# Kernel optimization log

Hardware: AMD Instinct MI355X
Metric: run time of the kernel (lower is better)

Reference implementation:

```python
import jax, jax.numpy as jnp
import numpy as np

BETA = 0.25
SCALE_NUM = 4  # len(latents_scale)


def setup_inputs() -> dict:
    key = jax.random.key(0)
    kz, ke = jax.random.split(key)
    z = jax.random.normal(kz, (8, 256, 32, 32), dtype=jnp.float32)
    emb_weight = jax.random.normal(ke, (16384, 256), dtype=jnp.float32) * 0.02
    return {"z": z, "emb_weight": emb_weight}


def reference(z, emb_weight):
    # z: [B, C, H, W] with C == vq_embed_dim and H == W (source reshapes with W twice)
    B, C, H, W = z.shape
    z_det = jax.lax.stop_gradient(z)

    # NOTE: in the source, `residual` is flattened ONCE before the scale loop and
    # never updated inside it, so every scale picks the same indices. We compute
    # the nearest-codebook assignment once (identical math, argmin of cdist is
    # invariant under sqrt, so squared distances suffice).
    residual = jnp.transpose(z_det, (0, 2, 3, 1)).reshape(-1, C)  # [N, D], N=B*H*W
    d2 = (jnp.sum(residual * residual, axis=1, keepdims=True)
          - 2.0 * residual @ emb_weight.T
          + jnp.sum(emb_weight * emb_weight, axis=1))  # [N, n_e]
    idx = jnp.argmin(d2, axis=1).reshape(B, W, W)  # [B, W, W]

    quantized = jnp.transpose(emb_weight[idx], (0, 3, 1, 2))  # [B, C, H, W]

    z_hat = jnp.zeros_like(z_det)
    loss = jnp.float32(0.0)
    for _ in range(SCALE_NUM):
        z_hat = z_hat + quantized
        loss = loss + BETA * jnp.mean((jax.lax.stop_gradient(z_hat) - z) ** 2) \
                    + jnp.mean((z_hat - z_det) ** 2)
    loss = loss / SCALE_NUM

    total_idx = jnp.concatenate([idx] * SCALE_NUM, axis=1)  # [B, SCALE_NUM*W, W]
    z_hat_out = z + jax.lax.stop_gradient(z_hat - z)  # straight-through
    return z_hat_out, loss, total_idx
```

## Files before the change

### kernel.cpp

```cpp
#include <hip/hip_runtime.h>

#define D      256
#define N_E    16384
#define NPTS   8192
#define ZOUT   2097152
#define MARGIN 2.0e-2f
#define STRIPS 4
#define ECH    17

typedef short bf16x8 __attribute__((ext_vector_type(8)));
typedef unsigned short us8 __attribute__((ext_vector_type(8)));
typedef float f32x16 __attribute__((ext_vector_type(16)));
typedef unsigned long long u64;

__device__ __forceinline__ unsigned short f2bf(float x) {
    unsigned int u = __float_as_uint(x);
    return (unsigned short)((u + 0x7FFFu + ((u >> 16) & 1u)) >> 16);
}
__device__ __forceinline__ float bf2f(unsigned short h) {
    return __uint_as_float((unsigned int)h << 16);
}
__device__ __forceinline__ void gl_lds16(const void* g, void* l) {
    __builtin_amdgcn_global_load_lds(
        (const __attribute__((address_space(1))) unsigned int*)g,
        (__attribute__((address_space(3))) unsigned int*)l, 16, 0, 0);
}

__global__ __launch_bounds__(256) void prep(
    const float* __restrict__ z, const float* __restrict__ emb,
    unsigned short* __restrict__ Zpk, float* __restrict__ Zf32,
    unsigned short* __restrict__ Epk, float* __restrict__ e2,
    float* __restrict__ loss) {
    __shared__ float sh[32];
    const int t = threadIdx.x;
    if (blockIdx.x == 0 && t == 0) loss[0] = 0.f;
    if (blockIdx.x < 256) {
        const int n0 = blockIdx.x * 32;
        const int p = t & 31, ks8 = t >> 5;
        const int n = n0 + p;
        const int b = n >> 10, hw = n & 1023;
        const float* zb = z + (size_t)b * 262144 + hw;
        const int k0 = ks8 * 32;
        float v[32];
        #pragma unroll
        for (int kk = 0; kk < 32; ++kk)
            v[kk] = zb[(size_t)(k0 + kk) * 1024];
        #pragma unroll
        for (int i = 0; i < 8; ++i) {
            float4 f = {v[i * 4], v[i * 4 + 1], v[i * 4 + 2], v[i * 4 + 3]};
            *(float4*)(Zf32 + (size_t)n * D + k0 + i * 4) = f;
        }
        const int g = n >> 5;
        #pragma unroll
        for (int i = 0; i < 4; ++i) {
            us8 hv;
            #pragma unroll
            for (int c = 0; c < 8; ++c) hv[c] = f2bf(-2.0f * v[i * 8 + c]);
            const int kabs = k0 + i * 8;
            const int ks = kabs >> 4;
            const int l = (n & 31) + ((kabs >> 3) & 1) * 32;
            *(us8*)(Zpk + ((size_t)(g * 16 + ks) * 64 + l) * 8) = hv;
        }
    } else {
        const int bi = blockIdx.x - 256;
        const int j0 = bi * 32;
        const int jj = j0 + (t >> 3), q = t & 7;
        const float* row = emb + (size_t)jj * D + q * 32;
        float v[32];
        float s = 0.f;
        #pragma unroll
        for (int i = 0; i < 8; ++i) {
            const float4 x = *(const float4*)(row + i * 4);
            v[i * 4] = x.x; v[i * 4 + 1] = x.y; v[i * 4 + 2] = x.z; v[i * 4 + 3] = x.w;
            s += x.x * x.x + x.y * x.y + x.z * x.z + x.w * x.w;
        }
        #pragma unroll
        for (int i = 0; i < 4; ++i) {
            us8 hv;
            #pragma unroll
            for (int c = 0; c < 8; ++c) hv[c] = f2bf(v[i * 8 + c]);
            const int kabs = q * 32 + i * 8;
            const int ks = kabs >> 4;
            const int l = (jj & 31) + ((kabs >> 3) & 1) * 32;
            *(us8*)(Epk + ((size_t)(bi * ECH + ks) * 64 + l) * 8) = hv;
        }
        s += __shfl_xor(s, 1);
        s += __shfl_xor(s, 2);
        s += __shfl_xor(s, 4);
        if (q == 0) { e2[jj] = s; sh[t >> 3] = s; }
        __syncthreads();
        if (t < 64) {
            us8 hv;
            #pragma unroll
            for (int c = 0; c < 8; ++c) hv[c] = 0;
            if (t < 32) {
                const float vv = sh[t];
                const unsigned short hi = f2bf(vv);
                hv[0] = hi;
                hv[1] = f2bf(vv - bf2f(hi));
            }
            *(us8*)(Epk + ((size_t)bi * ECH + 16) * 512 + t * 8) = hv;
        }
    }
}

__global__ __launch_bounds__(256, 2) void mfma_gemm(
    const unsigned short* __restrict__ Epk, const unsigned short* __restrict__ Zpk,
    float* __restrict__ tminv, u64* __restrict__ tmask) {
    __shared__ unsigned short Zbuf[64 * 512];

    const int tid = threadIdx.x, lane = tid & 63, wid = tid >> 6;
    const int c32 = lane & 31, l5 = lane >> 5;
    const int n0 = blockIdx.x * 128;
    const int cs0 = blockIdx.y * (STRIPS * 256);

    us8 puu;
    #pragma unroll
    for (int c = 0; c < 8; ++c) puu[c] = 0;
    if (l5 == 0) { puu[0] = 0x3F80; puu[1] = 0x3F80; }
    const bf16x8 pu = (bf16x8)puu;

    #pragma unroll
    for (int ks = 0; ks < 16; ++ks)
        gl_lds16(Zpk + ((size_t)((n0 >> 5) + wid) * 16 + ks) * 512 + lane * 8,
                 Zbuf + (wid * 16 + ks) * 512);
    __syncthreads();

    for (int s = 0; s < STRIPS; ++s) {
        const int cb = cs0 + s * 256 + wid * 64;
        const unsigned short* eb =
            Epk + ((size_t)(cb >> 5) * ECH) * 512 + lane * 8;
        const unsigned short* zb = Zbuf + lane * 8;

        f32x16 acc[2][4];
        const f32x16 z16 = {0.f};
        #pragma unroll
        for (int i = 0; i < 2; ++i)
            #pragma unroll
            for (int j = 0; j < 4; ++j) acc[i][j] = z16;

        bf16x8 eq0a = *(const bf16x8*)(eb);
        bf16x8 eq0b = *(const bf16x8*)(eb + ECH * 512);
        bf16x8 eq1a = *(const bf16x8*)(eb + 512);
        bf16x8 eq1b = *(const bf16x8*)(eb + ECH * 512 + 512);
        bf16x8 pc[4], pn[4];
        #pragma unroll
        for (int j = 0; j < 4; ++j) pc[j] = *(const bf16x8*)(zb + (j * 16) * 512);

        #pragma unroll 4
        for (int ks = 0; ks < 16; ++ks) {
            bf16x8 ef0, ef1;
            if ((ks & 1) == 0) { ef0 = eq0a; ef1 = eq0b; }
            else               { ef0 = eq1a; ef1 = eq1b; }
            if (ks < 15) {
                const unsigned short* ep = eb + (ks + 2) * 512;
                if ((ks & 1) == 0) {
                    eq0a = *(const bf16x8*)ep;
                    eq0b = *(const bf16x8*)(ep + ECH * 512);
                } else {
                    eq1a = *(const bf16x8*)ep;
                    eq1b = *(const bf16x8*)(ep + ECH * 512);
                }
                #pragma unroll
                for (int j = 0; j < 4; ++j)
                    pn[j] = *(const bf16x8*)(zb + (j * 16 + ks + 1) * 512);
            }
            acc[0][0] = __builtin_amdgcn_mfma_f32_32x32x16_bf16(ef0, pc[0], acc[0][0], 0, 0, 0);
            acc[0][1] = __builtin_amdgcn_mfma_f32_32x32x16_bf16(ef0, pc[1], acc[0][1], 0, 0, 0);
            acc[0][2] = __builtin_amdgcn_mfma_f32_32x32x16_bf16(ef0, pc[2], acc[0][2], 0, 0, 0);
            acc[0][3] = __builtin_amdgcn_mfma_f32_32x32x16_bf16(ef0, pc[3], acc[0][3], 0, 0, 0);
            acc[1][0] = __builtin_amdgcn_mfma_f32_32x32x16_bf16(ef1, pc[0], acc[1][0], 0, 0, 0);
            acc[1][1] = __builtin_amdgcn_mfma_f32_32x32x16_bf16(ef1, pc[1], acc[1][1], 0, 0, 0);
            acc[1][2] = __builtin_amdgcn_mfma_f32_32x32x16_bf16(ef1, pc[2], acc[1][2], 0, 0, 0);
            acc[1][3] = __builtin_amdgcn_mfma_f32_32x32x16_bf16(ef1, pc[3], acc[1][3], 0, 0, 0);
            if (ks < 15) {
                #pragma unroll
                for (int j = 0; j < 4; ++j) pc[j] = pn[j];
            }
        }
        #pragma unroll
        for (int j = 0; j < 4; ++j) {
            acc[0][j] = __builtin_amdgcn_mfma_f32_32x32x16_bf16(eq0a, pu, acc[0][j], 0, 0, 0);
            acc[1][j] = __builtin_amdgcn_mfma_f32_32x32x16_bf16(eq0b, pu, acc[1][j], 0, 0, 0);
        }

        #pragma unroll
        for (int j = 0; j < 4; ++j) {
            float m = acc[0][j][0];
            #pragma unroll
            for (int r = 1; r < 16; ++r) m = fminf(m, acc[0][j][r]);
            #pragma unroll
            for (int r = 0; r < 16; ++r) m = fminf(m, acc[1][j][r]);
            m = fminf(m, __shfl_xor(m, 32));
            const float th = m + MARGIN;
            unsigned mk[2];
            #pragma unroll
            for (int i = 0; i < 2; ++i) {
                unsigned mm = 0;
                #pragma unroll
                for (int r = 0; r < 16; ++r) {
                    const int row = (r & 3) + 8 * (r >> 2) + 4 * l5;
                    mm |= (acc[i][j][r] <= th) ? (1u << row) : 0u;
                }
                mk[i] = mm | (unsigned)__shfl_xor((int)mm, 32);
            }
            if (l5 == 0) {
                const size_t pt = (size_t)(n0 + j * 32 + c32);
                tminv[pt * 256 + (cb >> 6)] = m;
                tmask[pt * 256 + (cb >> 6)] = ((u64)mk[1] << 32) | (u64)mk[0];
            }
        }
    }
}

__global__ __launch_bounds__(1024) void rescore_quant(
    const float* __restrict__ tminv, const u64* __restrict__ tmask,
    const float* __restrict__ Zf32, const float* __restrict__ emb,
    const float* __restrict__ e2, const float* __restrict__ z,
    float* __restrict__ out, float* __restrict__ out_idx,
    float* __restrict__ loss) {
    __shared__ int idx_s[32];
    __shared__ float wsum[16];
    const int tid = threadIdx.x, lane = tid & 63, wd = tid >> 6;
    const int n0 = blockIdx.x * 32;
    const int b = n0 >> 10, hw0 = n0 & 1023;

    #pragma unroll 1
    for (int p = 0; p < 2; ++p) {
        const int lp = wd * 2 + p;
        const int n = n0 + lp;
        const float4 zr = *(const float4*)(Zf32 + (size_t)n * D + lane * 4);
        const float4 tv = *(const float4*)(tminv + (size_t)n * 256 + lane * 4);

        float m1 = fminf(fminf(tv.x, tv.y), fminf(tv.z, tv.w));
        #pragma unroll
        for (int st = 1; st < 64; st <<= 1) m1 = fminf(m1, __shfl_xor(m1, st));
        const float thresh = m1 + MARGIN;

        u64 best = ~0ull;
        const float tva[4] = {tv.x, tv.y, tv.z, tv.w};
        #pragma unroll
        for (int k = 0; k < 4; ++k) {
            u64 gm = __ballot(tva[k] <= thresh);
            while (gm) {
                const int bit = (int)__builtin_ctzll(gm);
                gm &= gm - 1;
                const int g = bit * 4 + k;
                u64 cm = tmask[(size_t)n * 256 + g];
                while (cm) {
                    const int r = (int)__builtin_ctzll(cm);
                    cm &= cm - 1;
                    const int c = g * 64 + r;
                    const float4 ev = *(const float4*)(emb + (size_t)c * D + lane * 4);
                    float s = zr.x * ev.x + zr.y * ev.y + zr.z * ev.z + zr.w * ev.w;
                    #pragma unroll
                    for (int st = 1; st < 64; st <<= 1) s += __shfl_xor(s, st);
                    const float d = e2[c] - 2.0f * s;
                    unsigned int u = __float_as_uint(d);
                    u = (u & 0x80000000u) ? ~u : (u | 0x80000000u);
                    const u64 key = ((u64)u << 32) | (unsigned int)c;
                    if (key < best) best = key;
                }
            }
        }
        if (lane == 0)
            idx_s[lp] = (int)(unsigned int)(best & 0xFFFFFFFFull);
    }
    __syncthreads();

    if (tid < 32) {
        const float fv = (float)idx_s[tid];
        #pragma unroll
        for (int sc = 0; sc < 4; ++sc)
            out_idx[b * 4096 + sc * 1024 + hw0 + tid] = fv;
    }
    const int hw_l = tid & 31, cg = tid >> 5;
    const int j = idx_s[hw_l];
    const float* er = emb + (size_t)j * D + cg * 8;
    const float4 q0 = *(const float4*)er;
    const float4 q1 = *(const float4*)(er + 4);
    const float qv[8] = {q0.x, q0.y, q0.z, q0.w, q1.x, q1.y, q1.z, q1.w};
    float e = 0.f;
    #pragma unroll
    for (int cc = 0; cc < 8; ++cc) {
        const int c = cg * 8 + cc;
        const size_t zi = (size_t)b * 262144 + (size_t)c * 1024 + hw0 + hw_l;
        const float zv = z[zi];
        const float q = qv[cc];
        const float zh = ((q + q) + q) + q;
        out[zi] = zv + (zh - zv);
        e += 30.0f * q * q - 20.0f * q * zv + 4.0f * zv * zv;
    }
    #pragma unroll
    for (int off = 32; off > 0; off >>= 1) e += __shfl_down(e, off);
    if (lane == 0) wsum[wd] = e;
    __syncthreads();
    if (tid == 0) {
        float s = 0.f;
        #pragma unroll
        for (int i = 0; i < 16; ++i) s += wsum[i];
        atomicAdd(loss, s * (0.3125f / 2097152.0f));
    }
}

extern "C" void kernel_launch(void* const* d_in, const int* in_sizes, int n_in,
                              void* d_out, int out_size, void* d_ws, size_t ws_size,
                              hipStream_t stream) {
    const float* z = (const float*)d_in[0];
    const float* emb = (const float*)d_in[1];
    float* out = (float*)d_out;

    unsigned short* Zpk = (unsigned short*)d_ws;
    unsigned short* Epk = Zpk + (size_t)NPTS * D;
    float* Zf32 = (float*)(Epk + (size_t)(N_E / 32) * ECH * 512);
    float* e2 = Zf32 + (size_t)NPTS * D;
    float* tminv = e2 + N_E;
    u64* tmask = (u64*)(tminv + (size_t)NPTS * 256);

    float* loss = out + ZOUT;
    float* out_idx = out + ZOUT + 1;

    prep<<<768, 256, 0, stream>>>(z, emb, Zpk, Zf32, Epk, e2, loss);
    mfma_gemm<<<dim3(NPTS / 128, N_E / (256 * STRIPS)), 256, 0, stream>>>(
        Epk, Zpk, tminv, tmask);
    rescore_quant<<<256, 1024, 0, stream>>>(tminv, tmask, Zf32, emb, e2, z,
                                            out, out_idx, loss);
}
```

Baseline: 161.6 us.

## Fuse GEMM and rescore kernels using a grid-wide atomic barrier

```diff
diff --git a/kernel.cpp b/kernel.cpp
--- a/kernel.cpp
+++ b/kernel.cpp
@@ -7,6 +7,7 @@
 #define MARGIN 2.0e-2f
 #define STRIPS 4
 #define ECH    17
+#define GRIDF  512
 
 typedef short bf16x8 __attribute__((ext_vector_type(8)));
 typedef unsigned short us8 __attribute__((ext_vector_type(8)));
@@ -30,10 +31,10 @@
     const float* __restrict__ z, const float* __restrict__ emb,
     unsigned short* __restrict__ Zpk, float* __restrict__ Zf32,
     unsigned short* __restrict__ Epk, float* __restrict__ e2,
-    float* __restrict__ loss) {
+    float* __restrict__ loss, unsigned int* __restrict__ cnt) {
     __shared__ float sh[32];
     const int t = threadIdx.x;
-    if (blockIdx.x == 0 && t == 0) loss[0] = 0.f;
+    if (blockIdx.x == 0 && t == 0) { loss[0] = 0.f; *cnt = 0u; }
     if (blockIdx.x < 256) {
         const int n0 = blockIdx.x * 32;
         const int p = t & 31, ks8 = t >> 5;
@@ -104,15 +105,22 @@
     }
 }
 
-__global__ __launch_bounds__(256, 2) void mfma_gemm(
+__global__ __launch_bounds__(256, 2) void gemm_fused(
     const unsigned short* __restrict__ Epk, const unsigned short* __restrict__ Zpk,
-    float* __restrict__ tminv, u64* __restrict__ tmask) {
+    float* __restrict__ tminv, u64* __restrict__ tmask,
+    const float* __restrict__ Zf32, const float* __restrict__ emb,
+    const float* __restrict__ e2, const float* __restrict__ z,
+    float* __restrict__ out, float* __restrict__ out_idx,
+    float* __restrict__ loss, unsigned int* __restrict__ cnt) {
     __shared__ unsigned short Zbuf[64 * 512];
+    __shared__ int idx_s[16];
+    __shared__ float wsum[4];
 
     const int tid = threadIdx.x, lane = tid & 63, wid = tid >> 6;
     const int c32 = lane & 31, l5 = lane >> 5;
-    const int n0 = blockIdx.x * 128;
-    const int cs0 = blockIdx.y * (STRIPS * 256);
+    const int bx = (int)blockIdx.x & 63;
+    const int byb = (int)blockIdx.x >> 6;
+    const int n0 = bx * 128;
 
     us8 puu;
     #pragma unroll
@@ -126,109 +134,113 @@
                  Zbuf + (wid * 16 + ks) * 512);
     __syncthreads();
 
-    for (int s = 0; s < STRIPS; ++s) {
-        const int cb = cs0 + s * 256 + wid * 64;
-        const unsigned short* eb =
-            Epk + ((size_t)(cb >> 5) * ECH) * 512 + lane * 8;
-        const unsigned short* zb = Zbuf + lane * 8;
-
-        f32x16 acc[2][4];
-        const f32x16 z16 = {0.f};
-        #pragma unroll
-        for (int i = 0; i < 2; ++i)
-            #pragma unroll
-            for (int j = 0; j < 4; ++j) acc[i][j] = z16;
-
-        bf16x8 eq0a = *(const bf16x8*)(eb);
-        bf16x8 eq0b = *(const bf16x8*)(eb + ECH * 512);
-        bf16x8 eq1a = *(const bf16x8*)(eb + 512);
-        bf16x8 eq1b = *(const bf16x8*)(eb + ECH * 512 + 512);
-        bf16x8 pc[4], pn[4];
-        #pragma unroll
-        for (int j = 0; j < 4; ++j) pc[j] = *(const bf16x8*)(zb + (j * 16) * 512);
-
-        #pragma unroll 4
-        for (int ks = 0; ks < 16; ++ks) {
-            bf16x8 ef0, ef1;
-            if ((ks & 1) == 0) { ef0 = eq0a; ef1 = eq0b; }
-            else               { ef0 = eq1a; ef1 = eq1b; }
-            if (ks < 15) {
-                const unsigned short* ep = eb + (ks + 2) * 512;
-                if ((ks & 1) == 0) {
-                    eq0a = *(const bf16x8*)ep;
-                    eq0b = *(const bf16x8*)(ep + ECH * 512);
-                } else {
-                    eq1a = *(const bf16x8*)ep;
-                    eq1b = *(const bf16x8*)(ep + ECH * 512);
-                }
+    #pragma unroll 1
+    for (int tyi = 0; tyi < 2; ++tyi) {
+        const int cs0 = (byb + tyi * 8) * (STRIPS * 256);
+        #pragma unroll 1
+        for (int s = 0; s < STRIPS; ++s) {
+            const int cb = cs0 + s * 256 + wid * 64;
+            const unsigned short* eb =
+                Epk + ((size_t)(cb >> 5) * ECH) * 512 + lane * 8;
+            const unsigned short* zb = Zbuf + lane * 8;
+
+            f32x16 acc[2][4];
+            const f32x16 z16 = {0.f};
+            #pragma unroll
+            for (int i = 0; i < 2; ++i)
                 #pragma unroll
-                for (int j = 0; j < 4; ++j)
-                    pn[j] = *(const bf16x8*)(zb + (j * 16 + ks + 1) * 512);
-            }
-            acc[0][0] = __builtin_amdgcn_mfma_f32_32x32x16_bf16(ef0, pc[0], acc[0][0], 0, 0, 0);
-            acc[0][1] = __builtin_amdgcn_mfma_f32_32x32x16_bf16(ef0, pc[1], acc[0][1], 0, 0, 0);
-            acc[0][2] = __builtin_amdgcn_mfma_f32_32x32x16_bf16(ef0, pc[2], acc[0][2], 0, 0, 0);
-            acc[0][3] = __builtin_amdgcn_mfma_f32_32x32x16_bf16(ef0, pc[3], acc[0][3], 0, 0, 0);
-            acc[1][0] = __builtin_amdgcn_mfma_f32_32x32x16_bf16(ef1, pc[0], acc[1][0], 0, 0, 0);
-            acc[1][1] = __builtin_amdgcn_mfma_f32_32x32x16_bf16(ef1, pc[1], acc[1][1], 0, 0, 0);
-            acc[1][2] = __builtin_amdgcn_mfma_f32_32x32x16_bf16(ef1, pc[2], acc[1][2], 0, 0, 0);
-            acc[1][3] = __builtin_amdgcn_mfma_f32_32x32x16_bf16(ef1, pc[3], acc[1][3], 0, 0, 0);
-            if (ks < 15) {
+                for (int j = 0; j < 4; ++j) acc[i][j] = z16;
+
+            bf16x8 eq0a = *(const bf16x8*)(eb);
+            bf16x8 eq0b = *(const bf16x8*)(eb + ECH * 512);
+            bf16x8 eq1a = *(const bf16x8*)(eb + 512);
+            bf16x8 eq1b = *(const bf16x8*)(eb + ECH * 512 + 512);
+            bf16x8 pc[4], pn[4];
+            #pragma unroll
+            for (int j = 0; j < 4; ++j)
+                pc[j] = *(const bf16x8*)(zb + (j * 16) * 512);
+
+            #pragma unroll 4
+            for (int ks = 0; ks < 16; ++ks) {
+                bf16x8 ef0, ef1;
+                if ((ks & 1) == 0) { ef0 = eq0a; ef1 = eq0b; }
+                else               { ef0 = eq1a; ef1 = eq1b; }
+                if (ks < 15) {
+                    const unsigned short* ep = eb + (ks + 2) * 512;
+                    if ((ks & 1) == 0) {
+                        eq0a = *(const bf16x8*)ep;
+                        eq0b = *(const bf16x8*)(ep + ECH * 512);
+                    } else {
+                        eq1a = *(const bf16x8*)ep;
+                        eq1b = *(const bf16x8*)(ep + ECH * 512);
+                    }
+                    #pragma unroll
+                    for (int j = 0; j < 4; ++j)
+                        pn[j] = *(const bf16x8*)(zb + (j * 16 + ks + 1) * 512);
+                }
+                acc[0][0] = __builtin_amdgcn_mfma_f32_32x32x16_bf16(ef0, pc[0], acc[0][0], 0, 0, 0);
+                acc[0][1] = __builtin_amdgcn_mfma_f32_32x32x16_bf16(ef0, pc[1], acc[0][1], 0, 0, 0);
+                acc[0][2] = __builtin_amdgcn_mfma_f32_32x32x16_bf16(ef0, pc[2], acc[0][2], 0, 0, 0);
+                acc[0][3] = __builtin_amdgcn_mfma_f32_32x32x16_bf16(ef0, pc[3], acc[0][3], 0, 0, 0);
+                acc[1][0] = __builtin_amdgcn_mfma_f32_32x32x16_bf16(ef1, pc[0], acc[1][0], 0, 0, 0);
+                acc[1][1] = __builtin_amdgcn_mfma_f32_32x32x16_bf16(ef1, pc[1], acc[1][1], 0, 0, 0);
+                acc[1][2] = __builtin_amdgcn_mfma_f32_32x32x16_bf16(ef1, pc[2], acc[1][2], 0, 0, 0);
+                acc[1][3] = __builtin_amdgcn_mfma_f32_32x32x16_bf16(ef1, pc[3], acc[1][3], 0, 0, 0);
+                if (ks < 15) {
+                    #pragma unroll
+                    for (int j = 0; j < 4; ++j) pc[j] = pn[j];
+                }
+            }
+            #pragma unroll
+            for (int j = 0; j < 4; ++j) {
+                acc[0][j] = __builtin_amdgcn_mfma_f32_32x32x16_bf16(eq0a, pu, acc[0][j], 0, 0, 0);
+                acc[1][j] = __builtin_amdgcn_mfma_f32_32x32x16_bf16(eq0b, pu, acc[1][j], 0, 0, 0);
+            }
+
+            #pragma unroll
+            for (int j = 0; j < 4; ++j) {
+                float m = acc[0][j][0];
                 #pragma unroll
-                for (int j = 0; j < 4; ++j) pc[j] = pn[j];
-            }
-        }
-        #pragma unroll
-        for (int j = 0; j < 4; ++j) {
-            acc[0][j] = __builtin_amdgcn_mfma_f32_32x32x16_bf16(eq0a, pu, acc[0][j], 0, 0, 0);
-            acc[1][j] = __builtin_amdgcn_mfma_f32_32x32x16_bf16(eq0b, pu, acc[1][j], 0, 0, 0);
-        }
-
-        #pragma unroll
-        for (int j = 0; j < 4; ++j) {
-            float m = acc[0][j][0];
-            #pragma unroll
-            for (int r = 1; r < 16; ++r) m = fminf(m, acc[0][j][r]);
-            #pragma unroll
-            for (int r = 0; r < 16; ++r) m = fminf(m, acc[1][j][r]);
-            m = fminf(m, __shfl_xor(m, 32));
-            const float th = m + MARGIN;
-            unsigned mk[2];
-            #pragma unroll
-            for (int i = 0; i < 2; ++i) {
-                unsigned mm = 0;
+                for (int r = 1; r < 16; ++r) m = fminf(m, acc[0][j][r]);
                 #pragma unroll
-                for (int r = 0; r < 16; ++r) {
-                    const int row = (r & 3) + 8 * (r >> 2) + 4 * l5;
-                    mm |= (acc[i][j][r] <= th) ? (1u << row) : 0u;
-                }
-                mk[i] = mm | (unsigned)__shfl_xor((int)mm, 32);
-            }
-            if (l5 == 0) {
-                const size_t pt = (size_t)(n0 + j * 32 + c32);
-                tminv[pt * 256 + (cb >> 6)] = m;
-                tmask[pt * 256 + (cb >> 6)] = ((u64)mk[1] << 32) | (u64)mk[0];
-            }
-        }
-    }
-}
-
-__global__ __launch_bounds__(1024) void rescore_quant(
-    const float* __restrict__ tminv, const u64* __restrict__ tmask,
-    const float* __restrict__ Zf32, const float* __restrict__ emb,
-    const float* __restrict__ e2, const float* __restrict__ z,
-    float* __restrict__ out, float* __restrict__ out_idx,
-    float* __restrict__ loss) {
-    __shared__ int idx_s[32];
-    __shared__ float wsum[16];
-    const int tid = threadIdx.x, lane = tid & 63, wd = tid >> 6;
-    const int n0 = blockIdx.x * 32;
-    const int b = n0 >> 10, hw0 = n0 & 1023;
-
+                for (int r = 0; r < 16; ++r) m = fminf(m, acc[1][j][r]);
+                m = fminf(m, __shfl_xor(m, 32));
+                const float th = m + MARGIN;
+                unsigned mk[2];
+                #pragma unroll
+                for (int i = 0; i < 2; ++i) {
+                    unsigned mm = 0;
+                    #pragma unroll
+                    for (int r = 0; r < 16; ++r) {
+                        const int row = (r & 3) + 8 * (r >> 2) + 4 * l5;
+                        mm |= (acc[i][j][r] <= th) ? (1u << row) : 0u;
+                    }
+                    mk[i] = mm | (unsigned)__shfl_xor((int)mm, 32);
+                }
+                if (l5 == 0) {
+                    const size_t pt = (size_t)(n0 + j * 32 + c32);
+                    tminv[pt * 256 + (cb >> 6)] = m;
+                    tmask[pt * 256 + (cb >> 6)] = ((u64)mk[1] << 32) | (u64)mk[0];
+                }
+            }
+        }
+    }
+
+    __threadfence();
+    __syncthreads();
+    if (tid == 0) {
+        atomicAdd(cnt, 1u);
+        while (atomicAdd(cnt, 0u) < GRIDF) __builtin_amdgcn_s_sleep(32);
+    }
+    __syncthreads();
+    __threadfence();
+
+    const int n0r = (int)blockIdx.x * 16;
+    const int br = n0r >> 10, hw0r = n0r & 1023;
     #pragma unroll 1
-    for (int p = 0; p < 2; ++p) {
-        const int lp = wd * 2 + p;
-        const int n = n0 + lp;
+    for (int p = 0; p < 4; ++p) {
+        const int lp = wid * 4 + p;
+        const int n = n0r + lp;
         const float4 zr = *(const float4*)(Zf32 + (size_t)n * D + lane * 4);
         const float4 tv = *(const float4*)(tminv + (size_t)n * 256 + lane * 4);
 
@@ -268,23 +280,27 @@
     }
     __syncthreads();
 
-    if (tid < 32) {
+    if (tid < 16) {
         const float fv = (float)idx_s[tid];
         #pragma unroll
         for (int sc = 0; sc < 4; ++sc)
-            out_idx[b * 4096 + sc * 1024 + hw0 + tid] = fv;
-    }
-    const int hw_l = tid & 31, cg = tid >> 5;
+            out_idx[br * 4096 + sc * 1024 + hw0r + tid] = fv;
+    }
+    const int hw_l = tid & 15, cg = tid >> 4;
     const int j = idx_s[hw_l];
-    const float* er = emb + (size_t)j * D + cg * 8;
-    const float4 q0 = *(const float4*)er;
-    const float4 q1 = *(const float4*)(er + 4);
-    const float qv[8] = {q0.x, q0.y, q0.z, q0.w, q1.x, q1.y, q1.z, q1.w};
+    const float* er = emb + (size_t)j * D + cg * 16;
+    float qv[16];
+    #pragma unroll
+    for (int i = 0; i < 4; ++i) {
+        const float4 q4 = *(const float4*)(er + i * 4);
+        qv[i * 4] = q4.x; qv[i * 4 + 1] = q4.y;
+        qv[i * 4 + 2] = q4.z; qv[i * 4 + 3] = q4.w;
+    }
     float e = 0.f;
     #pragma unroll
-    for (int cc = 0; cc < 8; ++cc) {
-        const int c = cg * 8 + cc;
-        const size_t zi = (size_t)b * 262144 + (size_t)c * 1024 + hw0 + hw_l;
+    for (int cc = 0; cc < 16; ++cc) {
+        const int c = cg * 16 + cc;
+        const size_t zi = (size_t)br * 262144 + (size_t)c * 1024 + hw0r + hw_l;
         const float zv = z[zi];
         const float q = qv[cc];
         const float zh = ((q + q) + q) + q;
@@ -293,12 +309,10 @@
     }
     #pragma unroll
     for (int off = 32; off > 0; off >>= 1) e += __shfl_down(e, off);
-    if (lane == 0) wsum[wd] = e;
+    if (lane == 0) wsum[wid] = e;
     __syncthreads();
     if (tid == 0) {
-        float s = 0.f;
-        #pragma unroll
-        for (int i = 0; i < 16; ++i) s += wsum[i];
+        const float s = wsum[0] + wsum[1] + wsum[2] + wsum[3];
         atomicAdd(loss, s * (0.3125f / 2097152.0f));
     }
 }
@@ -316,13 +330,12 @@
     float* e2 = Zf32 + (size_t)NPTS * D;
     float* tminv = e2 + N_E;
     u64* tmask = (u64*)(tminv + (size_t)NPTS * 256);
+    unsigned int* cnt = (unsigned int*)(tmask + (size_t)NPTS * 256);
 
     float* loss = out + ZOUT;
     float* out_idx = out + ZOUT + 1;
 
-    prep<<<768, 256, 0, stream>>>(z, emb, Zpk, Zf32, Epk, e2, loss);
-    mfma_gemm<<<dim3(NPTS / 128, N_E / (256 * STRIPS)), 256, 0, stream>>>(
-        Epk, Zpk, tminv, tmask);
-    rescore_quant<<<256, 1024, 0, stream>>>(tminv, tmask, Zf32, emb, e2, z,
-                                            out, out_idx, loss);
-}
+    prep<<<768, 256, 0, stream>>>(z, emb, Zpk, Zf32, Epk, e2, loss, cnt);
+    gemm_fused<<<GRIDF, 256, 0, stream>>>(Epk, Zpk, tminv, tmask, Zf32, emb,
+                                          e2, z, out, out_idx, loss, cnt);
+}
```

New measurement: 286.1 us. +77.1%, slower.

## Drop Zf32 scratch buffer and stage z tile in LDS; swap GEMM grid order

Applied to the files above, without the earlier changes.

```diff
diff --git a/kernel.cpp b/kernel.cpp
--- a/kernel.cpp
+++ b/kernel.cpp
@@ -28,9 +28,8 @@
 
 __global__ __launch_bounds__(256) void prep(
     const float* __restrict__ z, const float* __restrict__ emb,
-    unsigned short* __restrict__ Zpk, float* __restrict__ Zf32,
-    unsigned short* __restrict__ Epk, float* __restrict__ e2,
-    float* __restrict__ loss) {
+    unsigned short* __restrict__ Zpk, unsigned short* __restrict__ Epk,
+    float* __restrict__ e2, float* __restrict__ loss) {
     __shared__ float sh[32];
     const int t = threadIdx.x;
     if (blockIdx.x == 0 && t == 0) loss[0] = 0.f;
@@ -45,11 +44,6 @@
         #pragma unroll
         for (int kk = 0; kk < 32; ++kk)
             v[kk] = zb[(size_t)(k0 + kk) * 1024];
-        #pragma unroll
-        for (int i = 0; i < 8; ++i) {
-            float4 f = {v[i * 4], v[i * 4 + 1], v[i * 4 + 2], v[i * 4 + 3]};
-            *(float4*)(Zf32 + (size_t)n * D + k0 + i * 4) = f;
-        }
         const int g = n >> 5;
         #pragma unroll
         for (int i = 0; i < 4; ++i) {
@@ -111,8 +105,8 @@
 
     const int tid = threadIdx.x, lane = tid & 63, wid = tid >> 6;
     const int c32 = lane & 31, l5 = lane >> 5;
-    const int n0 = blockIdx.x * 128;
-    const int cs0 = blockIdx.y * (STRIPS * 256);
+    const int n0 = (int)blockIdx.y * 128;
+    const int cs0 = (int)blockIdx.x * (STRIPS * 256);
 
     us8 puu;
     #pragma unroll
@@ -215,21 +209,31 @@
 
 __global__ __launch_bounds__(1024) void rescore_quant(
     const float* __restrict__ tminv, const u64* __restrict__ tmask,
-    const float* __restrict__ Zf32, const float* __restrict__ emb,
-    const float* __restrict__ e2, const float* __restrict__ z,
-    float* __restrict__ out, float* __restrict__ out_idx,
-    float* __restrict__ loss) {
+    const float* __restrict__ emb, const float* __restrict__ e2,
+    const float* __restrict__ z, float* __restrict__ out,
+    float* __restrict__ out_idx, float* __restrict__ loss) {
+    __shared__ float smz[32][257];
     __shared__ int idx_s[32];
     __shared__ float wsum[16];
     const int tid = threadIdx.x, lane = tid & 63, wd = tid >> 6;
     const int n0 = blockIdx.x * 32;
     const int b = n0 >> 10, hw0 = n0 & 1023;
 
+    #pragma unroll
+    for (int pass = 0; pass < 8; ++pass) {
+        const int c = pass * 32 + (tid >> 5);
+        const int hw = tid & 31;
+        smz[hw][c] = z[(size_t)b * 262144 + (size_t)c * 1024 + hw0 + hw];
+    }
+    __syncthreads();
+
     #pragma unroll 1
     for (int p = 0; p < 2; ++p) {
         const int lp = wd * 2 + p;
         const int n = n0 + lp;
-        const float4 zr = *(const float4*)(Zf32 + (size_t)n * D + lane * 4);
+        const float* zrow = smz[lp];
+        const float4 zr = {zrow[lane * 4], zrow[lane * 4 + 1],
+                           zrow[lane * 4 + 2], zrow[lane * 4 + 3]};
         const float4 tv = *(const float4*)(tminv + (size_t)n * 256 + lane * 4);
 
         float m1 = fminf(fminf(tv.x, tv.y), fminf(tv.z, tv.w));
@@ -285,7 +289,7 @@
     for (int cc = 0; cc < 8; ++cc) {
         const int c = cg * 8 + cc;
         const size_t zi = (size_t)b * 262144 + (size_t)c * 1024 + hw0 + hw_l;
-        const float zv = z[zi];
+        const float zv = smz[hw_l][c];
         const float q = qv[cc];
         const float zh = ((q + q) + q) + q;
         out[zi] = zv + (zh - zv);
@@ -312,17 +316,16 @@
 
     unsigned short* Zpk = (unsigned short*)d_ws;
     unsigned short* Epk = Zpk + (size_t)NPTS * D;
-    float* Zf32 = (float*)(Epk + (size_t)(N_E / 32) * ECH * 512);
-    float* e2 = Zf32 + (size_t)NPTS * D;
+    float* e2 = (float*)(Epk + (size_t)(N_E / 32) * ECH * 512);
     float* tminv = e2 + N_E;
     u64* tmask = (u64*)(tminv + (size_t)NPTS * 256);
 
     float* loss = out + ZOUT;
     float* out_idx = out + ZOUT + 1;
 
-    prep<<<768, 256, 0, stream>>>(z, emb, Zpk, Zf32, Epk, e2, loss);
-    mfma_gemm<<<dim3(NPTS / 128, N_E / (256 * STRIPS)), 256, 0, stream>>>(
+    prep<<<768, 256, 0, stream>>>(z, emb, Zpk, Epk, e2, loss);
+    mfma_gemm<<<dim3(N_E / (256 * STRIPS), NPTS / 128), 256, 0, stream>>>(
         Epk, Zpk, tminv, tmask);
-    rescore_quant<<<256, 1024, 0, stream>>>(tminv, tmask, Zf32, emb, e2, z,
+    rescore_quant<<<256, 1024, 0, stream>>>(tminv, tmask, emb, e2, z,
                                             out, out_idx, loss);
 }
```

Result: no change. 159.8 us, median of 2 (-1.1%).
